# Performance work log

Measured on AMD Instinct MI355X. Metric: run time of the kernel, lower is better.

The kernel has to match this reference:

```python
import jax, jax.numpy as jnp
import numpy as np

N = 2048; E = 5; C = 2; W_IN = 256; W_OUT = 128; NUM_CLASS = 8; NT = 1024


def _norm(H, add):
    # faithful to GTN.norm: transpose, zero diagonal, (optionally add I),
    # row-degree-normalize (diag(deg^-1) @ H expressed as row scaling), transpose back
    Ht = H.T
    n = Ht.shape[0]
    eye = jnp.eye(n, dtype=Ht.dtype)
    Ht = Ht * (1.0 - eye)
    if add:
        Ht = Ht + eye
    deg = jnp.sum(Ht, axis=1)
    deg_inv = jnp.where(deg == 0, jnp.zeros_like(deg), 1.0 / deg)
    return (deg_inv[:, None] * Ht).T


def _gtconv(A_e, w):
    # A_e: [E, N, N]; w: [C, E]; softmax over edge types then weighted sum
    return jnp.einsum('ce,enm->cnm', jax.nn.softmax(w, axis=1), A_e)


def setup_inputs() -> dict:
    key = jax.random.key(0)
    ks = jax.random.split(key, 12)
    A = jax.random.uniform(ks[0], (N, N, E), dtype=jnp.float32)
    X = jax.random.uniform(ks[1], (N, W_IN), dtype=jnp.float32)  # BCE target, in [0,1]
    target_x = jax.random.randint(ks[2], (NT,), 0, N)
    target = jax.random.randint(ks[3], (NT,), 0, NUM_CLASS)
    w0a = 0.1 * jax.random.normal(ks[4], (C, E), dtype=jnp.float32)
    w0b = 0.1 * jax.random.normal(ks[5], (C, E), dtype=jnp.float32)
    w1a = 0.1 * jax.random.normal(ks[6], (C, E), dtype=jnp.float32)
    W = jax.random.normal(ks[7], (W_IN, W_OUT), dtype=jnp.float32) * (1.0 / np.sqrt(W_IN))
    W1 = jax.random.normal(ks[8], (W_OUT * C, W_OUT), dtype=jnp.float32) * (1.0 / np.sqrt(W_OUT * C))
    W2 = jax.random.normal(ks[9], (W_OUT * C, W_IN), dtype=jnp.float32) * (1.0 / np.sqrt(W_OUT * C))
    lin_w = jax.random.normal(ks[10], (NUM_CLASS, W_OUT), dtype=jnp.float32) * (1.0 / np.sqrt(W_OUT))
    lin_b = jnp.zeros((NUM_CLASS,), dtype=jnp.float32)
    return {"A": A, "X": X, "W": W, "W1": W1, "W2": W2, "lin_w": lin_w,
            "lin_b": lin_b, "w0a": w0a, "w0b": w0b, "w1a": w1a,
            "target_x": target_x, "target": target}


def reference(A, X, W, W1, W2, lin_w, lin_b, w0a, w0b, w1a, target_x, target):
    A_e = jnp.transpose(A, (2, 0, 1))          # [E, N, N]
    # layer 0 (first=True): H = conv1(A) @ conv2(A)
    a = _gtconv(A_e, w0a)                      # [C, N, N]
    b = _gtconv(A_e, w0b)
    H = jnp.einsum('cij,cjk->cik', a, b)
    # layer 1 (first=False): H = normalization(H) @ conv1(A)
    Hn = jax.vmap(lambda h: _norm(h, False))(H)
    a1 = _gtconv(A_e, w1a)
    H = jnp.einsum('cij,cjk->cik', Hn, a1)
    # per-channel GCN conv: relu(norm(H_c, add=True).T @ (X @ W)), concat on features
    XW = X @ W                                 # [N, w_out]
    Hn2 = jax.vmap(lambda h: _norm(h, True))(H)
    Xc = jax.nn.relu(jnp.einsum('cji,jd->cid', Hn2, XW))  # [C, N, w_out]
    n = X.shape[0]
    X_cat = jnp.transpose(Xc, (1, 0, 2)).reshape(n, -1)   # [N, C*w_out]
    # sum channels, then the two head GCN convs share norm(H_sum, add=True)
    Hs = _norm(jnp.sum(H, axis=0), True)
    X_r = Hs.T @ (X_cat @ W2)                  # [N, w_in]
    X_o = Hs.T @ (X_cat @ W1)                  # [N, w_out]
    y = X_o[target_x] @ lin_w.T + lin_b        # [NT, num_class]
    # clamp reconstruction into [0,1] via sigmoid on out-of-range entries
    X_r = jnp.where(X_r > 1, jax.nn.sigmoid(X_r), X_r)
    X_r = jnp.where(X_r < 0, jax.nn.sigmoid(X_r), X_r)
    p = jnp.clip(X_r, 1e-7, 1.0 - 1e-7)
    lossR = -jnp.mean(X * jnp.log(p) + (1.0 - X) * jnp.log1p(-p))
    logp = jax.nn.log_softmax(y, axis=-1)
    lossC = -jnp.mean(jnp.take_along_axis(logp, target[:, None], axis=1))
    loss = lossC + lossR
    Ws = (jax.lax.stop_gradient(jax.nn.softmax(w0a, axis=1)),
          jax.lax.stop_gradient(jax.nn.softmax(w0b, axis=1)),
          jax.lax.stop_gradient(jax.nn.softmax(w1a, axis=1)))
    return (loss, y, Ws, lossR)
```

## Files before the change

### kernel.cpp

```cpp
#include <hip/hip_runtime.h>
#include <hip/hip_bf16.h>
#include <math.h>

#define NDIM 2048
#define EDIM 5
#define CDIM 2
#define WIN 256
#define WOUT 128
#define NCLS 8
#define NTGT 1024
#define NN ((size_t)NDIM * NDIM)
#define HNSC 256.0f
#define HNSCI 0.00390625f

typedef __attribute__((ext_vector_type(8))) short short8v;
typedef __attribute__((ext_vector_type(4))) float float4v;
typedef __attribute__((ext_vector_type(8))) int int8v;
typedef __attribute__((ext_vector_type(4))) int int4v;
typedef __attribute__((ext_vector_type(2))) int int2v;

__device__ __forceinline__ void gl2lds16(const void* g, void* l) {
  __builtin_amdgcn_global_load_lds((__attribute__((address_space(1))) const unsigned int*)g,
                                   (__attribute__((address_space(3))) unsigned int*)l, 16, 0, 0);
}
__device__ __forceinline__ float bf2f(unsigned short u) {
  return __uint_as_float(((unsigned)u) << 16);
}
__device__ __forceinline__ unsigned short f2bf(float f) {
  __hip_bfloat16 h = __float2bfloat16(f);
  return *(unsigned short*)&h;
}
__device__ __forceinline__ unsigned int pk4fp8(float a, float b, float c, float d) {
  int w = __builtin_amdgcn_cvt_pk_fp8_f32(a, b, 0, false);
  return (unsigned int)__builtin_amdgcn_cvt_pk_fp8_f32(c, d, w, true);
}

#define N_XBF (NDIM * WIN)
#define N_WT (WIN * WOUT)
#define N_W12T (384 * WIN)
#define N_PREP (N_XBF + N_WT + N_W12T + CDIM * NDIM + 16 + 30)
__global__ __launch_bounds__(256) void wsum_mega_k(
    const float* __restrict__ A, const float* __restrict__ w0a,
    const float* __restrict__ w0b, const float* __restrict__ w1a,
    unsigned char* __restrict__ a_out, unsigned char* __restrict__ bT,
    unsigned char* __restrict__ a1T,
    float* __restrict__ acc, float* __restrict__ deg,
    const float* __restrict__ X, const float* __restrict__ W,
    const float* __restrict__ W1, const float* __restrict__ W2,
    __hip_bfloat16* __restrict__ Xbf, __hip_bfloat16* __restrict__ WTbf,
    __hip_bfloat16* __restrict__ W12Tbf,
    float* __restrict__ dout) {
  const int b = blockIdx.x;
  const int tid = threadIdx.x;
  if (b >= 4096) {
    int idx = (b - 4096) * 256 + tid;
    if (idx < N_XBF) { Xbf[idx] = __float2bfloat16(X[idx]); return; }
    idx -= N_XBF;
    if (idx < N_WT) {
      int d = idx >> 8, k = idx & 255;
      WTbf[idx] = __float2bfloat16(W[k * WOUT + d]);
      return;
    }
    idx -= N_WT;
    if (idx < N_W12T) {
      int j = idx >> 8, k = idx & 255;
      W12Tbf[idx] = __float2bfloat16(j < 128 ? W1[k * 128 + j] : W2[k * 256 + (j - 128)]);
      return;
    }
    idx -= N_W12T;
    if (idx < CDIM * NDIM) { deg[idx] = 0.f; return; }
    idx -= CDIM * NDIM;
    if (idx < 16) { acc[idx] = 0.f; return; }
    idx -= 16;
    if (idx < 30) {
      int m = idx / 10, rr = idx - m * 10, c = rr / 5, e = rr - c * 5;
      const float* src = (m == 0) ? w0a : (m == 1) ? w0b : w1a;
      float mx = -1e30f;
      for (int t = 0; t < 5; ++t) mx = fmaxf(mx, src[c * 5 + t]);
      float s = 0.f, ve = 0.f;
      for (int t = 0; t < 5; ++t) {
        float ex = expf(src[c * 5 + t] - mx);
        s += ex;
        if (t == e) ve = ex;
      }
      dout[1 + NTGT * NCLS + idx] = ve / s;
    }
    return;
  }
  __shared__ float swl[32];
  __shared__ float tb[CDIM][32][33];
  __shared__ float tc[CDIM][32][33];
  if (tid < 6) {
    int m = tid >> 1, c = tid & 1;
    const float* src = (m == 0) ? w0a : (m == 1) ? w0b : w1a;
    float mx = -1e30f;
    for (int e = 0; e < 5; ++e) mx = fmaxf(mx, src[c * 5 + e]);
    float ex[5]; float s = 0.f;
    for (int e = 0; e < 5; ++e) { ex[e] = expf(src[c * 5 + e] - mx); s += ex[e]; }
    for (int e = 0; e < 5; ++e) swl[m * 10 + c * 5 + e] = ex[e] / s;
  }
  __syncthreads();
  const int bx = (b & 63) * 32, by = (b >> 6) * 32;
  const int tx4 = tid & 7, ty = tid >> 3;
  const int n = by + ty, m0 = bx + tx4 * 4;
  const float* ap = A + ((size_t)n * NDIM + m0) * EDIM;
  float4 f0 = *(const float4*)(ap);
  float4 f1 = *(const float4*)(ap + 4);
  float4 f2 = *(const float4*)(ap + 8);
  float4 f3 = *(const float4*)(ap + 12);
  float4 f4 = *(const float4*)(ap + 16);
  float v[4][5] = {{f0.x, f0.y, f0.z, f0.w, f1.x},
                   {f1.y, f1.z, f1.w, f2.x, f2.y},
                   {f2.z, f2.w, f3.x, f3.y, f3.z},
                   {f3.w, f4.x, f4.y, f4.z, f4.w}};
#pragma unroll
  for (int c = 0; c < CDIM; ++c) {
    float sa[4], sb[4], sc[4];
#pragma unroll
    for (int t = 0; t < 4; ++t) {
      sa[t] = swl[c*5]*v[t][0] + swl[c*5+1]*v[t][1] + swl[c*5+2]*v[t][2] +
              swl[c*5+3]*v[t][3] + swl[c*5+4]*v[t][4];
      sb[t] = swl[10+c*5]*v[t][0] + swl[10+c*5+1]*v[t][1] + swl[10+c*5+2]*v[t][2] +
              swl[10+c*5+3]*v[t][3] + swl[10+c*5+4]*v[t][4];
      sc[t] = swl[20+c*5]*v[t][0] + swl[20+c*5+1]*v[t][1] + swl[20+c*5+2]*v[t][2] +
              swl[20+c*5+3]*v[t][3] + swl[20+c*5+4]*v[t][4];
      tb[c][ty][tx4 * 4 + t] = sb[t];
      tc[c][ty][tx4 * 4 + t] = sc[t];
    }
    *(unsigned int*)(a_out + c * NN + (size_t)n * NDIM + m0) =
        pk4fp8(sa[0], sa[1], sa[2], sa[3]);
  }
  __syncthreads();
  const int mm = bx + ty, nn0 = by + tx4 * 4;
#pragma unroll
  for (int c = 0; c < CDIM; ++c) {
    float b0 = tb[c][tx4*4+0][ty], b1 = tb[c][tx4*4+1][ty];
    float b2 = tb[c][tx4*4+2][ty], b3 = tb[c][tx4*4+3][ty];
    float c0 = tc[c][tx4*4+0][ty], c1 = tc[c][tx4*4+1][ty];
    float c2 = tc[c][tx4*4+2][ty], c3 = tc[c][tx4*4+3][ty];
    *(unsigned int*)(bT + c * NN + (size_t)mm * NDIM + nn0) = pk4fp8(b0, b1, b2, b3);
    *(unsigned int*)(a1T + c * NN + (size_t)mm * NDIM + nn0) = pk4fp8(c0, c1, c2, c3);
  }
}

__device__ __forceinline__ void fp8_gemm_body(
    const unsigned char* __restrict__ A, const unsigned char* __restrict__ B,
    __hip_bfloat16* __restrict__ Cp, float* __restrict__ csp,
    int K, int ldc, int row0, int col0,
    unsigned char* As, unsigned char* Bs) {
  const int tid = threadIdx.x;
  const int lane = tid & 63;
  const int wave = tid >> 6;
  const int wr = (wave >> 1) * 64;
  const int wc = (wave & 1) * 64;
  const int q = lane >> 4;
  const int r = lane & 15;

  float4v acc[4][4] = {};

  const int srow = lane >> 3;
  const int scol = ((lane & 7) ^ (srow & 7)) * 16;
  const int fsw = r & 15 & 7;

  for (int k0 = 0; k0 < K; k0 += 128) {
    __syncthreads();
#pragma unroll
    for (int s = 0; s < 4; ++s) {
      gl2lds16(A + (size_t)(row0 + s * 32 + wave * 8 + srow) * K + k0 + scol,
               As + s * 4096 + wave * 1024);
      gl2lds16(B + (size_t)(col0 + s * 32 + wave * 8 + srow) * K + k0 + scol,
               Bs + s * 4096 + wave * 1024);
    }
    __syncthreads();

    union { int8v v; int4v h[2]; } ua[4], ub[4];
#pragma unroll
    for (int i = 0; i < 4; ++i) {
      const unsigned char* pa = As + (size_t)(wr + i * 16 + r) * 128;
      const unsigned char* pb = Bs + (size_t)(wc + i * 16 + r) * 128;
      ua[i].h[0] = *(const int4v*)(pa + (((2 * q) ^ fsw) * 16));
      ua[i].h[1] = *(const int4v*)(pa + (((2 * q + 1) ^ fsw) * 16));
      ub[i].h[0] = *(const int4v*)(pb + (((2 * q) ^ fsw) * 16));
      ub[i].h[1] = *(const int4v*)(pb + (((2 * q + 1) ^ fsw) * 16));
    }
#pragma unroll
    for (int i = 0; i < 4; ++i)
#pragma unroll
      for (int j = 0; j < 4; ++j)
        acc[i][j] = __builtin_amdgcn_mfma_scale_f32_16x16x128_f8f6f4(
            ua[i].v, ub[j].v, acc[i][j], 0, 0, 0, 0x7F7F7F7F, 0, 0x7F7F7F7F);
  }

#pragma unroll
  for (int i = 0; i < 4; ++i) {
    int row = row0 + wr + i * 16 + q * 4;
#pragma unroll
    for (int j = 0; j < 4; ++j) {
      int col = col0 + wc + j * 16 + r;
#pragma unroll
      for (int e = 0; e < 4; ++e)
        Cp[(size_t)(row + e) * ldc + col] = __float2bfloat16(acc[i][j][e]);
    }
  }

  if (csp) {
#pragma unroll
    for (int j = 0; j < 4; ++j) {
      int col = col0 + wc + j * 16 + r;
      float s = 0.f;
#pragma unroll
      for (int i = 0; i < 4; ++i) {
        int rowb = row0 + wr + i * 16 + q * 4;
#pragma unroll
        for (int e = 0; e < 4; ++e)
          if (rowb + e != col) s += acc[i][j][e];
      }
      s += __shfl_xor(s, 16, 64);
      s += __shfl_xor(s, 32, 64);
      if (lane < 16) atomicAdd(&csp[col], s);
    }
  }
}

__device__ __forceinline__ void bf16_gemm_body(
    const __hip_bfloat16* __restrict__ A, const __hip_bfloat16* __restrict__ B,
    __hip_bfloat16* __restrict__ Cp, int K, int ldc, int row0, int col0,
    int kbeg, int kend, char* As, char* Bs) {
  const int tid = threadIdx.x;
  const int lane = tid & 63;
  const int wave = tid >> 6;
  const int wr = (wave >> 1) * 64;
  const int wc = (wave & 1) * 64;
  const int q = lane >> 4;
  const int r = lane & 15;

  float4v acc[4][4] = {};

  const int srow = lane >> 3;
  const int scol = ((lane & 7) ^ (srow & 7)) * 8;
  const int fsw = r & 7;

  for (int k0 = kbeg; k0 < kend; k0 += 64) {
    __syncthreads();
#pragma unroll
    for (int s = 0; s < 4; ++s) {
      gl2lds16(A + (size_t)(row0 + s * 32 + wave * 8 + srow) * K + k0 + scol,
               As + s * 4096 + wave * 1024);
      gl2lds16(B + (size_t)(col0 + s * 32 + wave * 8 + srow) * K + k0 + scol,
               Bs + s * 4096 + wave * 1024);
    }
    __syncthreads();
#pragma unroll
    for (int h = 0; h < 2; ++h) {
      short8v af[4], bf[4];
#pragma unroll
      for (int i = 0; i < 4; ++i) {
        af[i] = *(const short8v*)(As + (size_t)(wr + i * 16 + r) * 128 +
                                  (((h * 4 + q) ^ fsw) * 16));
        bf[i] = *(const short8v*)(Bs + (size_t)(wc + i * 16 + r) * 128 +
                                  (((h * 4 + q) ^ fsw) * 16));
      }
#pragma unroll
      for (int i = 0; i < 4; ++i)
#pragma unroll
        for (int j = 0; j < 4; ++j)
          acc[i][j] = __builtin_amdgcn_mfma_f32_16x16x32_bf16(af[i], bf[j], acc[i][j], 0, 0, 0);
    }
  }

#pragma unroll
  for (int i = 0; i < 4; ++i) {
    int row = row0 + wr + i * 16 + q * 4;
#pragma unroll
    for (int j = 0; j < 4; ++j) {
      int col = col0 + wc + j * 16 + r;
#pragma unroll
      for (int e = 0; e < 4; ++e)
        Cp[(size_t)(row + e) * ldc + col] = __float2bfloat16(acc[i][j][e]);
    }
  }
}

__global__ __launch_bounds__(256) void gemm1_xwt_k(
    const unsigned char* __restrict__ P_a, const unsigned char* __restrict__ P_bT,
    __hip_bfloat16* __restrict__ H_bf, float* __restrict__ deg,
    const __hip_bfloat16* __restrict__ WTbf, const __hip_bfloat16* __restrict__ Xbf,
    __hip_bfloat16* __restrict__ XWT) {
  __shared__ __align__(16) unsigned char smem[32768];
  const int z = blockIdx.z;
  if (z < 2) {
    fp8_gemm_body(P_a + (size_t)z * NN, P_bT + (size_t)z * NN,
                  H_bf + (size_t)z * NN, deg + (size_t)z * NDIM,
                  NDIM, NDIM, blockIdx.y * 128, blockIdx.x * 128,
                  smem, smem + 16384);
  } else {
    if (blockIdx.y != 0) return;
    bf16_gemm_body(WTbf, Xbf, XWT, WIN, NDIM, 0, blockIdx.x * 128,
                   0, WIN, (char*)smem, (char*)smem + 16384);
  }
}

__global__ __launch_bounds__(256) void gemm2_k(
    const unsigned char* __restrict__ P_a1T, const unsigned char* __restrict__ P_Hn,
    __hip_bfloat16* __restrict__ H1T_bf) {
  __shared__ __align__(16) unsigned char smem[32768];
  const int z = blockIdx.z;
  fp8_gemm_body(P_a1T + (size_t)z * NN, P_Hn + (size_t)z * NN,
                H1T_bf + (size_t)z * NN, nullptr,
                NDIM, NDIM, blockIdx.y * 128, blockIdx.x * 128,
                smem, smem + 16384);
}

__global__ __launch_bounds__(256) void mfma_bt_k(
    const __hip_bfloat16* __restrict__ Ab, const __hip_bfloat16* __restrict__ Bt,
    __hip_bfloat16* __restrict__ Cv, int K, int ldc,
    size_t sA, size_t sB, size_t sC, size_t sSplit, int nsplit) {
  __shared__ __align__(16) char smem[32768];
  const int batch = blockIdx.z / nsplit;
  const int split = blockIdx.z - batch * nsplit;
  const int kchunk = K / nsplit;
  bf16_gemm_body(Ab + (size_t)batch * sA, Bt + (size_t)batch * sB,
                 Cv + (size_t)batch * sC + (size_t)split * sSplit,
                 K, ldc, blockIdx.y * 128, blockIdx.x * 128,
                 split * kchunk, split * kchunk + kchunk,
                 smem, smem + 16384);
}

__global__ __launch_bounds__(256) void col_scale_k(const __hip_bfloat16* __restrict__ H,
                                                   const float* __restrict__ deg,
                                                   unsigned char* __restrict__ out) {
  size_t base = ((size_t)blockIdx.x * 256 + threadIdx.x) * 8;
  int c = (int)(base >> 22);
  int i = (int)((base >> 11) & (NDIM - 1));
  int j0 = (int)(base & (NDIM - 1));
  union { short8v v; unsigned short u[8]; } p;
  p.v = *(const short8v*)(H + base);
  float f[8];
#pragma unroll
  for (int t = 0; t < 8; ++t) {
    int j = j0 + t;
    float d = deg[c * NDIM + j];
    float inv = (d == 0.f) ? 0.f : HNSC / d;
    float v = (i == j) ? 0.f : bf2f(p.u[t]);
    f[t] = v * inv;
  }
  int2v o;
  o.x = (int)pk4fp8(f[0], f[1], f[2], f[3]);
  o.y = (int)pk4fp8(f[4], f[5], f[6], f[7]);
  *(int2v*)(out + base) = o;
}

__global__ __launch_bounds__(256) void rowmega_k(const __hip_bfloat16* __restrict__ H1T,
                                                 __hip_bfloat16* __restrict__ Hn2T,
                                                 __hip_bfloat16* __restrict__ HsT) {
  const int m = blockIdx.x;
  const int tid = threadIdx.x;
  const size_t rb = (size_t)m * NDIM + tid * 8;
  union { short8v v; unsigned short u[8]; } a0, a1;
  a0.v = *(const short8v*)(H1T + rb);
  a1.v = *(const short8v*)(H1T + NN + rb);
  float v0[8], v1[8];
  float s0 = 0.f, s1 = 0.f;
#pragma unroll
  for (int t = 0; t < 8; ++t) {
    v0[t] = bf2f(a0.u[t]) * HNSCI;
    v1[t] = bf2f(a1.u[t]) * HNSCI;
    s0 += v0[t]; s1 += v1[t];
  }
  __shared__ float ds[2];
  __shared__ float red[2][4];
  __shared__ float bc[3];
  if (tid == (m >> 3)) { ds[0] = v0[m & 7]; ds[1] = v1[m & 7]; }
  for (int off = 32; off > 0; off >>= 1) {
    s0 += __shfl_down(s0, off, 64);
    s1 += __shfl_down(s1, off, 64);
  }
  if ((tid & 63) == 0) { red[0][tid >> 6] = s0; red[1][tid >> 6] = s1; }
  __syncthreads();
  if (tid == 0) {
    float t0 = red[0][0] + red[0][1] + red[0][2] + red[0][3];
    float t1 = red[1][0] + red[1][1] + red[1][2] + red[1][3];
    float r0 = t0 - ds[0] + 1.f;
    float r1 = t1 - ds[1] + 1.f;
    float rs = t0 + t1 - ds[0] - ds[1] + 1.f;
    bc[0] = (r0 == 0.f) ? 0.f : 1.f / r0;
    bc[1] = (r1 == 0.f) ? 0.f : 1.f / r1;
    bc[2] = (rs == 0.f) ? 0.f : 1.f / rs;
  }
  __syncthreads();
  float i0 = bc[0], i1 = bc[1], is = bc[2];
  union { short8v v; unsigned short u[8]; } o0, o1, os;
#pragma unroll
  for (int t = 0; t < 8; ++t) {
    bool dg = (tid * 8 + t == m);
    o0.u[t] = f2bf((dg ? 1.f : v0[t]) * i0);
    o1.u[t] = f2bf((dg ? 1.f : v1[t]) * i1);
    os.u[t] = f2bf((dg ? 1.f : (v0[t] + v1[t])) * is);
  }
  *(short8v*)(Hn2T + rb) = o0.v;
  *(short8v*)(Hn2T + NN + rb) = o1.v;
  *(short8v*)(HsT + rb) = os.v;
}

__global__ __launch_bounds__(256) void reduce_relu_k(const __hip_bfloat16* __restrict__ P7,
                                                     __hip_bfloat16* __restrict__ Xcat) {
  int idx = blockIdx.x * 256 + threadIdx.x;
  int c = idx >> 18;
  int rem = idx & 262143;
  float s = 0.f;
#pragma unroll
  for (int sp = 0; sp < 8; ++sp)
    s += __bfloat162float(P7[(size_t)c * 2097152 + (size_t)sp * 262144 + rem]);
  int n = rem >> 7, d = rem & 127;
  Xcat[(size_t)n * 256 + (c << 7) + d] = __float2bfloat16(fmaxf(s, 0.f));
}

__global__ __launch_bounds__(256) void loss_mega_k(const __hip_bfloat16* __restrict__ P10,
                                                   const float* __restrict__ X,
                                                   const float* __restrict__ lin_w,
                                                   const float* __restrict__ lin_b,
                                                   const int* __restrict__ txs,
                                                   const int* __restrict__ tgt,
                                                   float* __restrict__ yout,
                                                   float* __restrict__ acc) {
  const int b = blockIdx.x;
  const int tid = threadIdx.x;
  if (b < 2048) {
    float xr = 0.f;
#pragma unroll
    for (int sp = 0; sp < 8; ++sp)
      xr += __bfloat162float(P10[(size_t)sp * 786432 + (size_t)b * 384 + 128 + tid]);
    if (xr > 1.f) xr = 1.f / (1.f + expf(-xr));
    if (xr < 0.f) xr = 1.f / (1.f + expf(-xr));
    float p = fminf(fmaxf(xr, 1e-7f), 1.f - 1e-7f);
    float xv = X[(size_t)b * WIN + tid];
    float t = xv * logf(p) + (1.f - xv) * log1pf(-p);
    for (int off = 32; off > 0; off >>= 1) t += __shfl_down(t, off, 64);
    __shared__ float red[4];
    if ((tid & 63) == 0) red[tid >> 6] = t;
    __syncthreads();
    if (tid == 0) atomicAdd(acc + 1, red[0] + red[1] + red[2] + red[3]);
    return;
  }
  const int t = b - 2048;
  __shared__ float xo[WOUT];
  __shared__ float ys[NCLS];
  int x = txs[t];
  if (tid < WOUT) {
    float s = 0.f;
#pragma unroll
    for (int sp = 0; sp < 8; ++sp)
      s += __bfloat162float(P10[(size_t)sp * 786432 + (size_t)x * 384 + tid]);
    xo[tid] = s;
  }
  __syncthreads();
  if (tid < NCLS) {
    float s = lin_b[tid];
    for (int d = 0; d < WOUT; ++d) s += xo[d] * lin_w[tid * WOUT + d];
    ys[tid] = s;
    yout[(size_t)t * NCLS + tid] = s;
  }
  __syncthreads();
  if (tid == 0) {
    float m = ys[0];
    for (int k = 1; k < NCLS; ++k) m = fmaxf(m, ys[k]);
    float se = 0.f;
    for (int k = 0; k < NCLS; ++k) se += expf(ys[k] - m);
    float lse = m + logf(se);
    atomicAdd(acc, lse - ys[tgt[t]]);
  }
}

__global__ void finalize_k(const float* __restrict__ acc, float* __restrict__ dout) {
  float lossC = acc[0] / (float)NTGT;
  float lossR = -acc[1] / (float)(NDIM * WIN);
  dout[0] = lossC + lossR;
  dout[1 + NTGT * NCLS + 30] = lossR;
}

extern "C" void kernel_launch(void* const* d_in, const int* in_sizes, int n_in,
                              void* d_out, int out_size, void* d_ws, size_t ws_size,
                              hipStream_t stream) {
  const float* A    = (const float*)d_in[0];
  const float* X    = (const float*)d_in[1];
  const float* W    = (const float*)d_in[2];
  const float* W1   = (const float*)d_in[3];
  const float* W2   = (const float*)d_in[4];
  const float* linw = (const float*)d_in[5];
  const float* linb = (const float*)d_in[6];
  const float* w0a  = (const float*)d_in[7];
  const float* w0b  = (const float*)d_in[8];
  const float* w1a  = (const float*)d_in[9];
  const int* txs    = (const int*)d_in[10];
  const int* tgt    = (const int*)d_in[11];
  float* dout = (float*)d_out;

  float* ws = (float*)d_ws;
  unsigned char* wb = (unsigned char*)d_ws;
  unsigned char* P_a   = wb;
  unsigned char* P_bT  = wb + 2 * NN;
  unsigned char* P_a1T = wb + 4 * NN;
  unsigned char* P_Hn  = wb + 6 * NN;
  __hip_bfloat16* H_bf   = (__hip_bfloat16*)(ws + 2 * NN);
  __hip_bfloat16* H1T_bf = (__hip_bfloat16*)(ws + 3 * NN);
  __hip_bfloat16* Hn2T   = (__hip_bfloat16*)(ws + 4 * NN);
  __hip_bfloat16* HsT    = (__hip_bfloat16*)(ws);
  float* sm   = ws + 5 * NN;
  float* acc   = sm;                 sm += 16;
  float* deg   = sm;                 sm += CDIM * NDIM;
  __hip_bfloat16* Xbf    = (__hip_bfloat16*)sm;  sm += N_XBF / 2;
  __hip_bfloat16* WTbf   = (__hip_bfloat16*)sm;  sm += N_WT / 2;
  __hip_bfloat16* W12Tbf = (__hip_bfloat16*)sm;  sm += N_W12T / 2;
  __hip_bfloat16* XWT    = (__hip_bfloat16*)sm;  sm += (size_t)WOUT * NDIM / 2;
  __hip_bfloat16* Xcat   = (__hip_bfloat16*)sm;  sm += (size_t)NDIM * 256 / 2;
  __hip_bfloat16* XC12T  = (__hip_bfloat16*)sm;  sm += (size_t)384 * NDIM / 2;
  __hip_bfloat16* P7bf   = (__hip_bfloat16*)sm;  sm += (size_t)16 * 262144 / 2;
  __hip_bfloat16* P10bf  = (__hip_bfloat16*)sm;  sm += (size_t)8 * 786432 / 2;

  dim3 blk256(256);

  wsum_mega_k<<<dim3(4096 + (N_PREP + 255) / 256), blk256, 0, stream>>>(
      A, w0a, w0b, w1a, P_a, P_bT, P_a1T, acc, deg, X, W, W1, W2,
      Xbf, WTbf, W12Tbf, dout);
  gemm1_xwt_k<<<dim3(16, 16, 3), blk256, 0, stream>>>(P_a, P_bT, H_bf, deg,
                                                      WTbf, Xbf, XWT);
  col_scale_k<<<dim3((unsigned)(2 * NN / 2048)), blk256, 0, stream>>>(H_bf, deg, P_Hn);
  gemm2_k<<<dim3(16, 16, 2), blk256, 0, stream>>>(P_a1T, P_Hn, H1T_bf);
  rowmega_k<<<dim3(NDIM), blk256, 0, stream>>>(H1T_bf, Hn2T, HsT);
  mfma_bt_k<<<dim3(1, 16, 16), blk256, 0, stream>>>(Hn2T, XWT, P7bf, NDIM, WOUT,
                                                    NN, 0, 2097152, 262144, 8);
  reduce_relu_k<<<dim3(2048), blk256, 0, stream>>>(P7bf, Xcat);
  mfma_bt_k<<<dim3(16, 3, 1), blk256, 0, stream>>>(W12Tbf, Xcat, XC12T, 256, NDIM,
                                                   0, 0, 0, 0, 1);
  mfma_bt_k<<<dim3(3, 16, 8), blk256, 0, stream>>>(HsT, XC12T, P10bf, NDIM, 384,
                                                   0, 0, 0, 786432, 8);
  loss_mega_k<<<dim3(2048 + NTGT), blk256, 0, stream>>>(P10bf, X, linw, linb, txs, tgt,
                                                        dout + 1, acc);
  finalize_k<<<dim3(1), dim3(1), 0, stream>>>(acc, dout);
}
```

Baseline: 289.3 us.

## Fuse all stages into one cooperative persistent kernel with grid syncs

```diff
diff --git a/kernel.cpp b/kernel.cpp
--- a/kernel.cpp
+++ b/kernel.cpp
@@ -1,6 +1,9 @@
 #include <hip/hip_runtime.h>
+#include <hip/hip_cooperative_groups.h>
 #include <hip/hip_bf16.h>
 #include <math.h>
+
+namespace cg = cooperative_groups;
 
 #define NDIM 2048
 #define EDIM 5
@@ -12,6 +15,7 @@
 #define NN ((size_t)NDIM * NDIM)
 #define HNSC 256.0f
 #define HNSCI 0.00390625f
+#define GRID 512
 
 typedef __attribute__((ext_vector_type(8))) short short8v;
 typedef __attribute__((ext_vector_type(4))) float float4v;
@@ -39,111 +43,9 @@
 #define N_WT (WIN * WOUT)
 #define N_W12T (384 * WIN)
 #define N_PREP (N_XBF + N_WT + N_W12T + CDIM * NDIM + 16 + 30)
-__global__ __launch_bounds__(256) void wsum_mega_k(
-    const float* __restrict__ A, const float* __restrict__ w0a,
-    const float* __restrict__ w0b, const float* __restrict__ w1a,
-    unsigned char* __restrict__ a_out, unsigned char* __restrict__ bT,
-    unsigned char* __restrict__ a1T,
-    float* __restrict__ acc, float* __restrict__ deg,
-    const float* __restrict__ X, const float* __restrict__ W,
-    const float* __restrict__ W1, const float* __restrict__ W2,
-    __hip_bfloat16* __restrict__ Xbf, __hip_bfloat16* __restrict__ WTbf,
-    __hip_bfloat16* __restrict__ W12Tbf,
-    float* __restrict__ dout) {
-  const int b = blockIdx.x;
-  const int tid = threadIdx.x;
-  if (b >= 4096) {
-    int idx = (b - 4096) * 256 + tid;
-    if (idx < N_XBF) { Xbf[idx] = __float2bfloat16(X[idx]); return; }
-    idx -= N_XBF;
-    if (idx < N_WT) {
-      int d = idx >> 8, k = idx & 255;
-      WTbf[idx] = __float2bfloat16(W[k * WOUT + d]);
-      return;
-    }
-    idx -= N_WT;
-    if (idx < N_W12T) {
-      int j = idx >> 8, k = idx & 255;
-      W12Tbf[idx] = __float2bfloat16(j < 128 ? W1[k * 128 + j] : W2[k * 256 + (j - 128)]);
-      return;
-    }
-    idx -= N_W12T;
-    if (idx < CDIM * NDIM) { deg[idx] = 0.f; return; }
-    idx -= CDIM * NDIM;
-    if (idx < 16) { acc[idx] = 0.f; return; }
-    idx -= 16;
-    if (idx < 30) {
-      int m = idx / 10, rr = idx - m * 10, c = rr / 5, e = rr - c * 5;
-      const float* src = (m == 0) ? w0a : (m == 1) ? w0b : w1a;
-      float mx = -1e30f;
-      for (int t = 0; t < 5; ++t) mx = fmaxf(mx, src[c * 5 + t]);
-      float s = 0.f, ve = 0.f;
-      for (int t = 0; t < 5; ++t) {
-        float ex = expf(src[c * 5 + t] - mx);
-        s += ex;
-        if (t == e) ve = ex;
-      }
-      dout[1 + NTGT * NCLS + idx] = ve / s;
-    }
-    return;
-  }
-  __shared__ float swl[32];
-  __shared__ float tb[CDIM][32][33];
-  __shared__ float tc[CDIM][32][33];
-  if (tid < 6) {
-    int m = tid >> 1, c = tid & 1;
-    const float* src = (m == 0) ? w0a : (m == 1) ? w0b : w1a;
-    float mx = -1e30f;
-    for (int e = 0; e < 5; ++e) mx = fmaxf(mx, src[c * 5 + e]);
-    float ex[5]; float s = 0.f;
-    for (int e = 0; e < 5; ++e) { ex[e] = expf(src[c * 5 + e] - mx); s += ex[e]; }
-    for (int e = 0; e < 5; ++e) swl[m * 10 + c * 5 + e] = ex[e] / s;
-  }
-  __syncthreads();
-  const int bx = (b & 63) * 32, by = (b >> 6) * 32;
-  const int tx4 = tid & 7, ty = tid >> 3;
-  const int n = by + ty, m0 = bx + tx4 * 4;
-  const float* ap = A + ((size_t)n * NDIM + m0) * EDIM;
-  float4 f0 = *(const float4*)(ap);
-  float4 f1 = *(const float4*)(ap + 4);
-  float4 f2 = *(const float4*)(ap + 8);
-  float4 f3 = *(const float4*)(ap + 12);
-  float4 f4 = *(const float4*)(ap + 16);
-  float v[4][5] = {{f0.x, f0.y, f0.z, f0.w, f1.x},
-                   {f1.y, f1.z, f1.w, f2.x, f2.y},
-                   {f2.z, f2.w, f3.x, f3.y, f3.z},
-                   {f3.w, f4.x, f4.y, f4.z, f4.w}};
-#pragma unroll
-  for (int c = 0; c < CDIM; ++c) {
-    float sa[4], sb[4], sc[4];
-#pragma unroll
-    for (int t = 0; t < 4; ++t) {
-      sa[t] = swl[c*5]*v[t][0] + swl[c*5+1]*v[t][1] + swl[c*5+2]*v[t][2] +
-              swl[c*5+3]*v[t][3] + swl[c*5+4]*v[t][4];
-      sb[t] = swl[10+c*5]*v[t][0] + swl[10+c*5+1]*v[t][1] + swl[10+c*5+2]*v[t][2] +
-              swl[10+c*5+3]*v[t][3] + swl[10+c*5+4]*v[t][4];
-      sc[t] = swl[20+c*5]*v[t][0] + swl[20+c*5+1]*v[t][1] + swl[20+c*5+2]*v[t][2] +
-              swl[20+c*5+3]*v[t][3] + swl[20+c*5+4]*v[t][4];
-      tb[c][ty][tx4 * 4 + t] = sb[t];
-      tc[c][ty][tx4 * 4 + t] = sc[t];
-    }
-    *(unsigned int*)(a_out + c * NN + (size_t)n * NDIM + m0) =
-        pk4fp8(sa[0], sa[1], sa[2], sa[3]);
-  }
-  __syncthreads();
-  const int mm = bx + ty, nn0 = by + tx4 * 4;
-#pragma unroll
-  for (int c = 0; c < CDIM; ++c) {
-    float b0 = tb[c][tx4*4+0][ty], b1 = tb[c][tx4*4+1][ty];
-    float b2 = tb[c][tx4*4+2][ty], b3 = tb[c][tx4*4+3][ty];
-    float c0 = tc[c][tx4*4+0][ty], c1 = tc[c][tx4*4+1][ty];
-    float c2 = tc[c][tx4*4+2][ty], c3 = tc[c][tx4*4+3][ty];
-    *(unsigned int*)(bT + c * NN + (size_t)mm * NDIM + nn0) = pk4fp8(b0, b1, b2, b3);
-    *(unsigned int*)(a1T + c * NN + (size_t)mm * NDIM + nn0) = pk4fp8(c0, c1, c2, c3);
-  }
-}
-
-__device__ __forceinline__ void fp8_gemm_body(
+#define N_PREPB ((N_PREP + 255) / 256)
+
+__device__ void fp8_gemm_body(
     const unsigned char* __restrict__ A, const unsigned char* __restrict__ B,
     __hip_bfloat16* __restrict__ Cp, float* __restrict__ csp,
     int K, int ldc, int row0, int col0,
@@ -160,7 +62,7 @@
 
   const int srow = lane >> 3;
   const int scol = ((lane & 7) ^ (srow & 7)) * 16;
-  const int fsw = r & 15 & 7;
+  const int fsw = r & 7;
 
   for (int k0 = 0; k0 < K; k0 += 128) {
     __syncthreads();
@@ -222,7 +124,7 @@
   }
 }
 
-__device__ __forceinline__ void bf16_gemm_body(
+__device__ void bf16_gemm_body(
     const __hip_bfloat16* __restrict__ A, const __hip_bfloat16* __restrict__ B,
     __hip_bfloat16* __restrict__ Cp, int K, int ldc, int row0, int col0,
     int kbeg, int kend, char* As, char* Bs) {
@@ -281,201 +183,345 @@
   }
 }
 
-__global__ __launch_bounds__(256) void gemm1_xwt_k(
-    const unsigned char* __restrict__ P_a, const unsigned char* __restrict__ P_bT,
-    __hip_bfloat16* __restrict__ H_bf, float* __restrict__ deg,
-    const __hip_bfloat16* __restrict__ WTbf, const __hip_bfloat16* __restrict__ Xbf,
-    __hip_bfloat16* __restrict__ XWT) {
+__device__ void phase_exec(
+    int ph, int vb, unsigned char* smem,
+    const float* __restrict__ A, const float* __restrict__ X,
+    const float* __restrict__ W, const float* __restrict__ W1,
+    const float* __restrict__ W2, const float* __restrict__ linw,
+    const float* __restrict__ linb, const float* __restrict__ w0a,
+    const float* __restrict__ w0b, const float* __restrict__ w1a,
+    const int* __restrict__ txs, const int* __restrict__ tgt,
+    float* __restrict__ dout, float* __restrict__ ws) {
+  const int tid = threadIdx.x;
+  unsigned char* wb = (unsigned char*)ws;
+  unsigned char* P_a   = wb;
+  unsigned char* P_bT  = wb + 2 * NN;
+  unsigned char* P_a1T = wb + 4 * NN;
+  unsigned char* P_Hn  = wb + 6 * NN;
+  __hip_bfloat16* H_bf   = (__hip_bfloat16*)(ws + 2 * NN);
+  __hip_bfloat16* H1T_bf = (__hip_bfloat16*)(ws + 3 * NN);
+  __hip_bfloat16* Hn2T   = (__hip_bfloat16*)(ws + 4 * NN);
+  __hip_bfloat16* HsT    = (__hip_bfloat16*)(ws);
+  float* sm = ws + 5 * NN;
+  float* acc = sm;                sm += 16;
+  float* deg = sm;                sm += CDIM * NDIM;
+  __hip_bfloat16* Xbf    = (__hip_bfloat16*)sm;  sm += N_XBF / 2;
+  __hip_bfloat16* WTbf   = (__hip_bfloat16*)sm;  sm += N_WT / 2;
+  __hip_bfloat16* W12Tbf = (__hip_bfloat16*)sm;  sm += N_W12T / 2;
+  __hip_bfloat16* XWT    = (__hip_bfloat16*)sm;  sm += (size_t)WOUT * NDIM / 2;
+  __hip_bfloat16* Xcat   = (__hip_bfloat16*)sm;  sm += (size_t)NDIM * 256 / 2;
+  __hip_bfloat16* XC12T  = (__hip_bfloat16*)sm;  sm += (size_t)384 * NDIM / 2;
+  __hip_bfloat16* P7bf   = (__hip_bfloat16*)sm;  sm += (size_t)16 * 262144 / 2;
+  __hip_bfloat16* P10bf  = (__hip_bfloat16*)sm;  sm += (size_t)8 * 786432 / 2;
+
+  switch (ph) {
+    case 0: {
+      if (vb >= 4096) {
+        int idx = (vb - 4096) * 256 + tid;
+        if (idx < N_XBF) { Xbf[idx] = __float2bfloat16(X[idx]); break; }
+        idx -= N_XBF;
+        if (idx < N_WT) {
+          int d = idx >> 8, k = idx & 255;
+          WTbf[idx] = __float2bfloat16(W[k * WOUT + d]);
+          break;
+        }
+        idx -= N_WT;
+        if (idx < N_W12T) {
+          int j = idx >> 8, k = idx & 255;
+          W12Tbf[idx] = __float2bfloat16(j < 128 ? W1[k * 128 + j] : W2[k * 256 + (j - 128)]);
+          break;
+        }
+        idx -= N_W12T;
+        if (idx < CDIM * NDIM) { deg[idx] = 0.f; break; }
+        idx -= CDIM * NDIM;
+        if (idx < 16) { acc[idx] = 0.f; break; }
+        idx -= 16;
+        if (idx < 30) {
+          int m = idx / 10, rr = idx - m * 10, c = rr / 5, e = rr - c * 5;
+          const float* src = (m == 0) ? w0a : (m == 1) ? w0b : w1a;
+          float mx = -1e30f;
+          for (int t = 0; t < 5; ++t) mx = fmaxf(mx, src[c * 5 + t]);
+          float s = 0.f, ve = 0.f;
+          for (int t = 0; t < 5; ++t) {
+            float ex = expf(src[c * 5 + t] - mx);
+            s += ex;
+            if (t == e) ve = ex;
+          }
+          dout[1 + NTGT * NCLS + idx] = ve / s;
+        }
+        break;
+      }
+      float* swl = (float*)smem;
+      float (*tb)[32][33] = (float(*)[32][33])(smem + 128);
+      float (*tc)[32][33] = (float(*)[32][33])(smem + 128 + 8448);
+      if (tid < 6) {
+        int m = tid >> 1, c = tid & 1;
+        const float* src = (m == 0) ? w0a : (m == 1) ? w0b : w1a;
+        float mx = -1e30f;
+        for (int e = 0; e < 5; ++e) mx = fmaxf(mx, src[c * 5 + e]);
+        float ex[5]; float s = 0.f;
+        for (int e = 0; e < 5; ++e) { ex[e] = expf(src[c * 5 + e] - mx); s += ex[e]; }
+        for (int e = 0; e < 5; ++e) swl[m * 10 + c * 5 + e] = ex[e] / s;
+      }
+      __syncthreads();
+      const int bx = (vb & 63) * 32, by = (vb >> 6) * 32;
+      const int tx4 = tid & 7, ty = tid >> 3;
+      const int n = by + ty, m0 = bx + tx4 * 4;
+      const float* ap = A + ((size_t)n * NDIM + m0) * EDIM;
+      float4 f0 = *(const float4*)(ap);
+      float4 f1 = *(const float4*)(ap + 4);
+      float4 f2 = *(const float4*)(ap + 8);
+      float4 f3 = *(const float4*)(ap + 12);
+      float4 f4 = *(const float4*)(ap + 16);
+      float v[4][5] = {{f0.x, f0.y, f0.z, f0.w, f1.x},
+                       {f1.y, f1.z, f1.w, f2.x, f2.y},
+                       {f2.z, f2.w, f3.x, f3.y, f3.z},
+                       {f3.w, f4.x, f4.y, f4.z, f4.w}};
+#pragma unroll
+      for (int c = 0; c < CDIM; ++c) {
+        float sa[4];
+#pragma unroll
+        for (int t = 0; t < 4; ++t) {
+          sa[t] = swl[c*5]*v[t][0] + swl[c*5+1]*v[t][1] + swl[c*5+2]*v[t][2] +
+                  swl[c*5+3]*v[t][3] + swl[c*5+4]*v[t][4];
+          tb[c][ty][tx4 * 4 + t] =
+              swl[10+c*5]*v[t][0] + swl[10+c*5+1]*v[t][1] + swl[10+c*5+2]*v[t][2] +
+              swl[10+c*5+3]*v[t][3] + swl[10+c*5+4]*v[t][4];
+          tc[c][ty][tx4 * 4 + t] =
+              swl[20+c*5]*v[t][0] + swl[20+c*5+1]*v[t][1] + swl[20+c*5+2]*v[t][2] +
+              swl[20+c*5+3]*v[t][3] + swl[20+c*5+4]*v[t][4];
+        }
+        *(unsigned int*)(P_a + c * NN + (size_t)n * NDIM + m0) =
+            pk4fp8(sa[0], sa[1], sa[2], sa[3]);
+      }
+      __syncthreads();
+      const int mm = bx + ty, nn0 = by + tx4 * 4;
+#pragma unroll
+      for (int c = 0; c < CDIM; ++c) {
+        *(unsigned int*)(P_bT + c * NN + (size_t)mm * NDIM + nn0) =
+            pk4fp8(tb[c][tx4*4+0][ty], tb[c][tx4*4+1][ty],
+                   tb[c][tx4*4+2][ty], tb[c][tx4*4+3][ty]);
+        *(unsigned int*)(P_a1T + c * NN + (size_t)mm * NDIM + nn0) =
+            pk4fp8(tc[c][tx4*4+0][ty], tc[c][tx4*4+1][ty],
+                   tc[c][tx4*4+2][ty], tc[c][tx4*4+3][ty]);
+      }
+      __syncthreads();
+      break;
+    }
+    case 1: {
+      if (vb < 512) {
+        int c = vb >> 8, x = vb & 15, y = (vb >> 4) & 15;
+        fp8_gemm_body(P_a + (size_t)c * NN, P_bT + (size_t)c * NN,
+                      H_bf + (size_t)c * NN, deg + (size_t)c * NDIM,
+                      NDIM, NDIM, y * 128, x * 128, smem, smem + 16384);
+      } else {
+        int x = vb - 512;
+        bf16_gemm_body(WTbf, Xbf, XWT, WIN, NDIM, 0, x * 128, 0, WIN,
+                       (char*)smem, (char*)smem + 16384);
+      }
+      break;
+    }
+    case 2: {
+      size_t base = ((size_t)vb * 256 + tid) * 8;
+      int c = (int)(base >> 22);
+      int i = (int)((base >> 11) & (NDIM - 1));
+      int j0 = (int)(base & (NDIM - 1));
+      union { short8v v; unsigned short u[8]; } p;
+      p.v = *(const short8v*)(H_bf + base);
+      float f[8];
+#pragma unroll
+      for (int t = 0; t < 8; ++t) {
+        int j = j0 + t;
+        float d = deg[c * NDIM + j];
+        float inv = (d == 0.f) ? 0.f : HNSC / d;
+        float vv = (i == j) ? 0.f : bf2f(p.u[t]);
+        f[t] = vv * inv;
+      }
+      int2v o;
+      o.x = (int)pk4fp8(f[0], f[1], f[2], f[3]);
+      o.y = (int)pk4fp8(f[4], f[5], f[6], f[7]);
+      *(int2v*)(P_Hn + base) = o;
+      break;
+    }
+    case 3: {
+      int c = vb >> 8, x = vb & 15, y = (vb >> 4) & 15;
+      fp8_gemm_body(P_a1T + (size_t)c * NN, P_Hn + (size_t)c * NN,
+                    H1T_bf + (size_t)c * NN, nullptr,
+                    NDIM, NDIM, y * 128, x * 128, smem, smem + 16384);
+      break;
+    }
+    case 4: {
+      const int m = vb;
+      float* ds = (float*)smem;
+      float* red = (float*)smem + 2;
+      float* bc = (float*)smem + 10;
+      const size_t rb = (size_t)m * NDIM + tid * 8;
+      union { short8v v; unsigned short u[8]; } a0, a1;
+      a0.v = *(const short8v*)(H1T_bf + rb);
+      a1.v = *(const short8v*)(H1T_bf + NN + rb);
+      float v0[8], v1[8];
+      float s0 = 0.f, s1 = 0.f;
+#pragma unroll
+      for (int t = 0; t < 8; ++t) {
+        v0[t] = bf2f(a0.u[t]) * HNSCI;
+        v1[t] = bf2f(a1.u[t]) * HNSCI;
+        s0 += v0[t]; s1 += v1[t];
+      }
+      if (tid == (m >> 3)) { ds[0] = v0[m & 7]; ds[1] = v1[m & 7]; }
+      for (int off = 32; off > 0; off >>= 1) {
+        s0 += __shfl_down(s0, off, 64);
+        s1 += __shfl_down(s1, off, 64);
+      }
+      if ((tid & 63) == 0) { red[tid >> 6] = s0; red[4 + (tid >> 6)] = s1; }
+      __syncthreads();
+      if (tid == 0) {
+        float t0 = red[0] + red[1] + red[2] + red[3];
+        float t1 = red[4] + red[5] + red[6] + red[7];
+        float r0 = t0 - ds[0] + 1.f;
+        float r1 = t1 - ds[1] + 1.f;
+        float rs = t0 + t1 - ds[0] - ds[1] + 1.f;
+        bc[0] = (r0 == 0.f) ? 0.f : 1.f / r0;
+        bc[1] = (r1 == 0.f) ? 0.f : 1.f / r1;
+        bc[2] = (rs == 0.f) ? 0.f : 1.f / rs;
+      }
+      __syncthreads();
+      float i0 = bc[0], i1 = bc[1], is = bc[2];
+      union { short8v v; unsigned short u[8]; } o0, o1, os;
+#pragma unroll
+      for (int t = 0; t < 8; ++t) {
+        bool dg = (tid * 8 + t == m);
+        o0.u[t] = f2bf((dg ? 1.f : v0[t]) * i0);
+        o1.u[t] = f2bf((dg ? 1.f : v1[t]) * i1);
+        os.u[t] = f2bf((dg ? 1.f : (v0[t] + v1[t])) * is);
+      }
+      *(short8v*)(Hn2T + rb) = o0.v;
+      *(short8v*)(Hn2T + NN + rb) = o1.v;
+      *(short8v*)(HsT + rb) = os.v;
+      __syncthreads();
+      break;
+    }
+    case 5: {
+      int c = vb >> 7, s = (vb >> 4) & 7, y = vb & 15;
+      bf16_gemm_body(Hn2T + (size_t)c * NN, XWT,
+                     P7bf + (size_t)c * 2097152 + (size_t)s * 262144,
+                     NDIM, WOUT, y * 128, 0, s * 256, s * 256 + 256,
+                     (char*)smem, (char*)smem + 16384);
+      break;
+    }
+    case 6: {
+      int idx = vb * 256 + tid;
+      int c = idx >> 18;
+      int rem = idx & 262143;
+      float s = 0.f;
+#pragma unroll
+      for (int sp = 0; sp < 8; ++sp)
+        s += __bfloat162float(P7bf[(size_t)c * 2097152 + (size_t)sp * 262144 + rem]);
+      int n = rem >> 7, d = rem & 127;
+      Xcat[(size_t)n * 256 + (c << 7) + d] = __float2bfloat16(fmaxf(s, 0.f));
+      break;
+    }
+    case 7: {
+      int x = vb & 15, y = vb >> 4;
+      bf16_gemm_body(W12Tbf, Xcat, XC12T, 256, NDIM, y * 128, x * 128, 0, 256,
+                     (char*)smem, (char*)smem + 16384);
+      break;
+    }
+    case 8: {
+      int z = vb / 48, rem = vb - z * 48;
+      int y = rem / 3, x = rem - y * 3;
+      bf16_gemm_body(HsT, XC12T, P10bf + (size_t)z * 786432,
+                     NDIM, 384, y * 128, x * 128, z * 256, z * 256 + 256,
+                     (char*)smem, (char*)smem + 16384);
+      break;
+    }
+    case 9: {
+      const int b = vb;
+      if (b < 2048) {
+        float xr = 0.f;
+#pragma unroll
+        for (int sp = 0; sp < 8; ++sp)
+          xr += __bfloat162float(P10bf[(size_t)sp * 786432 + (size_t)b * 384 + 128 + tid]);
+        if (xr > 1.f) xr = 1.f / (1.f + expf(-xr));
+        if (xr < 0.f) xr = 1.f / (1.f + expf(-xr));
+        float p = fminf(fmaxf(xr, 1e-7f), 1.f - 1e-7f);
+        float xv = X[(size_t)b * WIN + tid];
+        float t = xv * logf(p) + (1.f - xv) * log1pf(-p);
+        for (int off = 32; off > 0; off >>= 1) t += __shfl_down(t, off, 64);
+        float* red = (float*)smem;
+        if ((tid & 63) == 0) red[tid >> 6] = t;
+        __syncthreads();
+        if (tid == 0) atomicAdd(acc + 1, red[0] + red[1] + red[2] + red[3]);
+        __syncthreads();
+        break;
+      }
+      const int t = b - 2048;
+      float* xo = (float*)smem;
+      float* ys = (float*)smem + 128;
+      int x = txs[t];
+      if (tid < WOUT) {
+        float s = 0.f;
+#pragma unroll
+        for (int sp = 0; sp < 8; ++sp)
+          s += __bfloat162float(P10bf[(size_t)sp * 786432 + (size_t)x * 384 + tid]);
+        xo[tid] = s;
+      }
+      __syncthreads();
+      if (tid < NCLS) {
+        float s = linb[tid];
+        for (int d = 0; d < WOUT; ++d) s += xo[d] * linw[tid * WOUT + d];
+        ys[tid] = s;
+        dout[1 + (size_t)t * NCLS + tid] = s;
+      }
+      __syncthreads();
+      if (tid == 0) {
+        float m = ys[0];
+        for (int k = 1; k < NCLS; ++k) m = fmaxf(m, ys[k]);
+        float se = 0.f;
+        for (int k = 0; k < NCLS; ++k) se += expf(ys[k] - m);
+        float lse = m + logf(se);
+        atomicAdd(acc, lse - ys[tgt[t]]);
+      }
+      __syncthreads();
+      break;
+    }
+    case 10: {
+      if (vb == 0 && tid == 0) {
+        float lossC = acc[0] / (float)NTGT;
+        float lossR = -acc[1] / (float)(NDIM * WIN);
+        dout[0] = lossC + lossR;
+        dout[1 + NTGT * NCLS + 30] = lossR;
+      }
+      break;
+    }
+  }
+}
+
+__device__ __constant__ const int kPhaseCounts[11] = {
+    4096 + N_PREPB, 528, 4096, 512, 2048, 256, 2048, 48, 384, 3072, 1};
+
+__global__ __launch_bounds__(256, 2) void mega_k(
+    const float* A, const float* X, const float* W, const float* W1,
+    const float* W2, const float* linw, const float* linb, const float* w0a,
+    const float* w0b, const float* w1a, const int* txs, const int* tgt,
+    float* dout, float* ws) {
   __shared__ __align__(16) unsigned char smem[32768];
-  const int z = blockIdx.z;
-  if (z < 2) {
-    fp8_gemm_body(P_a + (size_t)z * NN, P_bT + (size_t)z * NN,
-                  H_bf + (size_t)z * NN, deg + (size_t)z * NDIM,
-                  NDIM, NDIM, blockIdx.y * 128, blockIdx.x * 128,
-                  smem, smem + 16384);
-  } else {
-    if (blockIdx.y != 0) return;
-    bf16_gemm_body(WTbf, Xbf, XWT, WIN, NDIM, 0, blockIdx.x * 128,
-                   0, WIN, (char*)smem, (char*)smem + 16384);
-  }
-}
-
-__global__ __launch_bounds__(256) void gemm2_k(
-    const unsigned char* __restrict__ P_a1T, const unsigned char* __restrict__ P_Hn,
-    __hip_bfloat16* __restrict__ H1T_bf) {
+  cg::grid_group grid = cg::this_grid();
+  for (int ph = 0; ph < 11; ++ph) {
+    for (int vb = blockIdx.x; vb < kPhaseCounts[ph]; vb += GRID)
+      phase_exec(ph, vb, smem, A, X, W, W1, W2, linw, linb, w0a, w0b, w1a,
+                 txs, tgt, dout, ws);
+    if (ph < 10) grid.sync();
+  }
+}
+
+__global__ __launch_bounds__(256, 2) void phase_k(
+    int ph, const float* A, const float* X, const float* W, const float* W1,
+    const float* W2, const float* linw, const float* linb, const float* w0a,
+    const float* w0b, const float* w1a, const int* txs, const int* tgt,
+    float* dout, float* ws) {
   __shared__ __align__(16) unsigned char smem[32768];
-  const int z = blockIdx.z;
-  fp8_gemm_body(P_a1T + (size_t)z * NN, P_Hn + (size_t)z * NN,
-                H1T_bf + (size_t)z * NN, nullptr,
-                NDIM, NDIM, blockIdx.y * 128, blockIdx.x * 128,
-                smem, smem + 16384);
-}
-
-__global__ __launch_bounds__(256) void mfma_bt_k(
-    const __hip_bfloat16* __restrict__ Ab, const __hip_bfloat16* __restrict__ Bt,
-    __hip_bfloat16* __restrict__ Cv, int K, int ldc,
-    size_t sA, size_t sB, size_t sC, size_t sSplit, int nsplit) {
-  __shared__ __align__(16) char smem[32768];
-  const int batch = blockIdx.z / nsplit;
-  const int split = blockIdx.z - batch * nsplit;
-  const int kchunk = K / nsplit;
-  bf16_gemm_body(Ab + (size_t)batch * sA, Bt + (size_t)batch * sB,
-                 Cv + (size_t)batch * sC + (size_t)split * sSplit,
-                 K, ldc, blockIdx.y * 128, blockIdx.x * 128,
-                 split * kchunk, split * kchunk + kchunk,
-                 smem, smem + 16384);
-}
-
-__global__ __launch_bounds__(256) void col_scale_k(const __hip_bfloat16* __restrict__ H,
-                                                   const float* __restrict__ deg,
-                                                   unsigned char* __restrict__ out) {
-  size_t base = ((size_t)blockIdx.x * 256 + threadIdx.x) * 8;
-  int c = (int)(base >> 22);
-  int i = (int)((base >> 11) & (NDIM - 1));
-  int j0 = (int)(base & (NDIM - 1));
-  union { short8v v; unsigned short u[8]; } p;
-  p.v = *(const short8v*)(H + base);
-  float f[8];
-#pragma unroll
-  for (int t = 0; t < 8; ++t) {
-    int j = j0 + t;
-    float d = deg[c * NDIM + j];
-    float inv = (d == 0.f) ? 0.f : HNSC / d;
-    float v = (i == j) ? 0.f : bf2f(p.u[t]);
-    f[t] = v * inv;
-  }
-  int2v o;
-  o.x = (int)pk4fp8(f[0], f[1], f[2], f[3]);
-  o.y = (int)pk4fp8(f[4], f[5], f[6], f[7]);
-  *(int2v*)(out + base) = o;
-}
-
-__global__ __launch_bounds__(256) void rowmega_k(const __hip_bfloat16* __restrict__ H1T,
-                                                 __hip_bfloat16* __restrict__ Hn2T,
-                                                 __hip_bfloat16* __restrict__ HsT) {
-  const int m = blockIdx.x;
-  const int tid = threadIdx.x;
-  const size_t rb = (size_t)m * NDIM + tid * 8;
-  union { short8v v; unsigned short u[8]; } a0, a1;
-  a0.v = *(const short8v*)(H1T + rb);
-  a1.v = *(const short8v*)(H1T + NN + rb);
-  float v0[8], v1[8];
-  float s0 = 0.f, s1 = 0.f;
-#pragma unroll
-  for (int t = 0; t < 8; ++t) {
-    v0[t] = bf2f(a0.u[t]) * HNSCI;
-    v1[t] = bf2f(a1.u[t]) * HNSCI;
-    s0 += v0[t]; s1 += v1[t];
-  }
-  __shared__ float ds[2];
-  __shared__ float red[2][4];
-  __shared__ float bc[3];
-  if (tid == (m >> 3)) { ds[0] = v0[m & 7]; ds[1] = v1[m & 7]; }
-  for (int off = 32; off > 0; off >>= 1) {
-    s0 += __shfl_down(s0, off, 64);
-    s1 += __shfl_down(s1, off, 64);
-  }
-  if ((tid & 63) == 0) { red[0][tid >> 6] = s0; red[1][tid >> 6] = s1; }
-  __syncthreads();
-  if (tid == 0) {
-    float t0 = red[0][0] + red[0][1] + red[0][2] + red[0][3];
-    float t1 = red[1][0] + red[1][1] + red[1][2] + red[1][3];
-    float r0 = t0 - ds[0] + 1.f;
-    float r1 = t1 - ds[1] + 1.f;
-    float rs = t0 + t1 - ds[0] - ds[1] + 1.f;
-    bc[0] = (r0 == 0.f) ? 0.f : 1.f / r0;
-    bc[1] = (r1 == 0.f) ? 0.f : 1.f / r1;
-    bc[2] = (rs == 0.f) ? 0.f : 1.f / rs;
-  }
-  __syncthreads();
-  float i0 = bc[0], i1 = bc[1], is = bc[2];
-  union { short8v v; unsigned short u[8]; } o0, o1, os;
-#pragma unroll
-  for (int t = 0; t < 8; ++t) {
-    bool dg = (tid * 8 + t == m);
-    o0.u[t] = f2bf((dg ? 1.f : v0[t]) * i0);
-    o1.u[t] = f2bf((dg ? 1.f : v1[t]) * i1);
-    os.u[t] = f2bf((dg ? 1.f : (v0[t] + v1[t])) * is);
-  }
-  *(short8v*)(Hn2T + rb) = o0.v;
-  *(short8v*)(Hn2T + NN + rb) = o1.v;
-  *(short8v*)(HsT + rb) = os.v;
-}
-
-__global__ __launch_bounds__(256) void reduce_relu_k(const __hip_bfloat16* __restrict__ P7,
-                                                     __hip_bfloat16* __restrict__ Xcat) {
-  int idx = blockIdx.x * 256 + threadIdx.x;
-  int c = idx >> 18;
-  int rem = idx & 262143;
-  float s = 0.f;
-#pragma unroll
-  for (int sp = 0; sp < 8; ++sp)
-    s += __bfloat162float(P7[(size_t)c * 2097152 + (size_t)sp * 262144 + rem]);
-  int n = rem >> 7, d = rem & 127;
-  Xcat[(size_t)n * 256 + (c << 7) + d] = __float2bfloat16(fmaxf(s, 0.f));
-}
-
-__global__ __launch_bounds__(256) void loss_mega_k(const __hip_bfloat16* __restrict__ P10,
-                                                   const float* __restrict__ X,
-                                                   const float* __restrict__ lin_w,
-                                                   const float* __restrict__ lin_b,
-                                                   const int* __restrict__ txs,
-                                                   const int* __restrict__ tgt,
-                                                   float* __restrict__ yout,
-                                                   float* __restrict__ acc) {
-  const int b = blockIdx.x;
-  const int tid = threadIdx.x;
-  if (b < 2048) {
-    float xr = 0.f;
-#pragma unroll
-    for (int sp = 0; sp < 8; ++sp)
-      xr += __bfloat162float(P10[(size_t)sp * 786432 + (size_t)b * 384 + 128 + tid]);
-    if (xr > 1.f) xr = 1.f / (1.f + expf(-xr));
-    if (xr < 0.f) xr = 1.f / (1.f + expf(-xr));
-    float p = fminf(fmaxf(xr, 1e-7f), 1.f - 1e-7f);
-    float xv = X[(size_t)b * WIN + tid];
-    float t = xv * logf(p) + (1.f - xv) * log1pf(-p);
-    for (int off = 32; off > 0; off >>= 1) t += __shfl_down(t, off, 64);
-    __shared__ float red[4];
-    if ((tid & 63) == 0) red[tid >> 6] = t;
-    __syncthreads();
-    if (tid == 0) atomicAdd(acc + 1, red[0] + red[1] + red[2] + red[3]);
-    return;
-  }
-  const int t = b - 2048;
-  __shared__ float xo[WOUT];
-  __shared__ float ys[NCLS];
-  int x = txs[t];
-  if (tid < WOUT) {
-    float s = 0.f;
-#pragma unroll
-    for (int sp = 0; sp < 8; ++sp)
-      s += __bfloat162float(P10[(size_t)sp * 786432 + (size_t)x * 384 + tid]);
-    xo[tid] = s;
-  }
-  __syncthreads();
-  if (tid < NCLS) {
-    float s = lin_b[tid];
-    for (int d = 0; d < WOUT; ++d) s += xo[d] * lin_w[tid * WOUT + d];
-    ys[tid] = s;
-    yout[(size_t)t * NCLS + tid] = s;
-  }
-  __syncthreads();
-  if (tid == 0) {
-    float m = ys[0];
-    for (int k = 1; k < NCLS; ++k) m = fmaxf(m, ys[k]);
-    float se = 0.f;
-    for (int k = 0; k < NCLS; ++k) se += expf(ys[k] - m);
-    float lse = m + logf(se);
-    atomicAdd(acc, lse - ys[tgt[t]]);
-  }
-}
-
-__global__ void finalize_k(const float* __restrict__ acc, float* __restrict__ dout) {
-  float lossC = acc[0] / (float)NTGT;
-  float lossR = -acc[1] / (float)(NDIM * WIN);
-  dout[0] = lossC + lossR;
-  dout[1 + NTGT * NCLS + 30] = lossR;
+  phase_exec(ph, blockIdx.x, smem, A, X, W, W1, W2, linw, linb, w0a, w0b, w1a,
+             txs, tgt, dout, ws);
 }
 
 extern "C" void kernel_launch(void* const* d_in, const int* in_sizes, int n_in,
@@ -494,47 +540,17 @@
   const int* txs    = (const int*)d_in[10];
   const int* tgt    = (const int*)d_in[11];
   float* dout = (float*)d_out;
-
   float* ws = (float*)d_ws;
-  unsigned char* wb = (unsigned char*)d_ws;
-  unsigned char* P_a   = wb;
-  unsigned char* P_bT  = wb + 2 * NN;
-  unsigned char* P_a1T = wb + 4 * NN;
-  unsigned char* P_Hn  = wb + 6 * NN;
-  __hip_bfloat16* H_bf   = (__hip_bfloat16*)(ws + 2 * NN);
-  __hip_bfloat16* H1T_bf = (__hip_bfloat16*)(ws + 3 * NN);
-  __hip_bfloat16* Hn2T   = (__hip_bfloat16*)(ws + 4 * NN);
-  __hip_bfloat16* HsT    = (__hip_bfloat16*)(ws);
-  float* sm   = ws + 5 * NN;
-  float* acc   = sm;                 sm += 16;
-  float* deg   = sm;                 sm += CDIM * NDIM;
-  __hip_bfloat16* Xbf    = (__hip_bfloat16*)sm;  sm += N_XBF / 2;
-  __hip_bfloat16* WTbf   = (__hip_bfloat16*)sm;  sm += N_WT / 2;
-  __hip_bfloat16* W12Tbf = (__hip_bfloat16*)sm;  sm += N_W12T / 2;
-  __hip_bfloat16* XWT    = (__hip_bfloat16*)sm;  sm += (size_t)WOUT * NDIM / 2;
-  __hip_bfloat16* Xcat   = (__hip_bfloat16*)sm;  sm += (size_t)NDIM * 256 / 2;
-  __hip_bfloat16* XC12T  = (__hip_bfloat16*)sm;  sm += (size_t)384 * NDIM / 2;
-  __hip_bfloat16* P7bf   = (__hip_bfloat16*)sm;  sm += (size_t)16 * 262144 / 2;
-  __hip_bfloat16* P10bf  = (__hip_bfloat16*)sm;  sm += (size_t)8 * 786432 / 2;
-
-  dim3 blk256(256);
-
-  wsum_mega_k<<<dim3(4096 + (N_PREP + 255) / 256), blk256, 0, stream>>>(
-      A, w0a, w0b, w1a, P_a, P_bT, P_a1T, acc, deg, X, W, W1, W2,
-      Xbf, WTbf, W12Tbf, dout);
-  gemm1_xwt_k<<<dim3(16, 16, 3), blk256, 0, stream>>>(P_a, P_bT, H_bf, deg,
-                                                      WTbf, Xbf, XWT);
-  col_scale_k<<<dim3((unsigned)(2 * NN / 2048)), blk256, 0, stream>>>(H_bf, deg, P_Hn);
-  gemm2_k<<<dim3(16, 16, 2), blk256, 0, stream>>>(P_a1T, P_Hn, H1T_bf);
-  rowmega_k<<<dim3(NDIM), blk256, 0, stream>>>(H1T_bf, Hn2T, HsT);
-  mfma_bt_k<<<dim3(1, 16, 16), blk256, 0, stream>>>(Hn2T, XWT, P7bf, NDIM, WOUT,
-                                                    NN, 0, 2097152, 262144, 8);
-  reduce_relu_k<<<dim3(2048), blk256, 0, stream>>>(P7bf, Xcat);
-  mfma_bt_k<<<dim3(16, 3, 1), blk256, 0, stream>>>(W12Tbf, Xcat, XC12T, 256, NDIM,
-                                                   0, 0, 0, 0, 1);
-  mfma_bt_k<<<dim3(3, 16, 8), blk256, 0, stream>>>(HsT, XC12T, P10bf, NDIM, 384,
-                                                   0, 0, 0, 786432, 8);
-  loss_mega_k<<<dim3(2048 + NTGT), blk256, 0, stream>>>(P10bf, X, linw, linb, txs, tgt,
-                                                        dout + 1, acc);
-  finalize_k<<<dim3(1), dim3(1), 0, stream>>>(acc, dout);
-}
+
+  void* args[] = {&A, &X, &W, &W1, &W2, &linw, &linb, &w0a, &w0b, &w1a,
+                  &txs, &tgt, &dout, &ws};
+  hipError_t err = hipLaunchCooperativeKernel((const void*)mega_k, dim3(GRID),
+                                              dim3(256), args, 0, stream);
+  if (err != hipSuccess) {
+    const int counts[11] = {4096 + N_PREPB, 528, 4096, 512, 2048, 256, 2048,
+                            48, 384, 3072, 1};
+    for (int ph = 0; ph < 11; ++ph)
+      phase_k<<<dim3(counts[ph]), dim3(256), 0, stream>>>(
+          ph, A, X, W, W1, W2, linw, linb, w0a, w0b, w1a, txs, tgt, dout, ws);
+  }
+}
```

After: 1.031 ms. 256% more time.
